# Kernel optimization log

Measured on AMD Instinct MI355X. Metric: run time of the kernel, lower is better.

## Reference

```python
import math
import jax, jax.numpy as jnp
import numpy as np

N = 2048          # batch size
D = 256           # embedding_dim
MEM = 16384       # memory_size
ANOMALY_WEIGHT = 1.0
TEMP = 0.1
MOMENTUM = 0.01
NCLS = 2          # binary phishing labels -> max(labels.max()+1, 2) == 2


def setup_inputs() -> dict:
    key = jax.random.key(0)
    ks = jax.random.split(key, 10)
    s = 1.0 / math.sqrt(D)  # nn.Linear default init range
    return {
        'z': jax.random.normal(ks[0], (N, D), jnp.float32),
        'labels': jax.random.randint(ks[1], (N,), 0, NCLS),
        'memory': jax.random.normal(ks[2], (MEM, D), jnp.float32),
        'memory_weights': jax.random.uniform(ks[3], (MEM,), jnp.float32),
        'running_mean': jnp.zeros((D,), jnp.float32),
        'running_cov': jnp.eye(D, dtype=jnp.float32),
        'Wq': jax.random.uniform(ks[4], (D, D), jnp.float32, -s, s),
        'bq': jax.random.uniform(ks[5], (D,), jnp.float32, -s, s),
        'Wk': jax.random.uniform(ks[6], (D, D), jnp.float32, -s, s),
        'bk': jax.random.uniform(ks[7], (D,), jnp.float32, -s, s),
        'Wv': jax.random.uniform(ks[8], (D, D), jnp.float32, -s, s),
        'bv': jax.random.uniform(ks[9], (D,), jnp.float32, -s, s),
    }


def reference(z, labels, memory, memory_weights, running_mean, running_cov,
              Wq, bq, Wk, bk, Wv, bv):
    # ---- update(z.detach(), labels): entire update path is detached in torch ----
    z_sg = jax.lax.stop_gradient(z)

    # _update_stats: EMA of batch mean / covariance (done before importance)
    mu = z_sg.mean(axis=0)                                  # [D]
    zc = z_sg - mu
    cov = zc.T @ zc / max(N - 1, 1)                         # [D, D]
    rm = (1.0 - MOMENTUM) * running_mean + MOMENTUM * mu
    rc = (1.0 - MOMENTUM) * running_cov + MOMENTUM * cov

    # _mahalanobis with updated running stats
    c = z_sg - rm
    cov_inv = jnp.linalg.inv(rc + 1e-6 * jnp.eye(D, dtype=rc.dtype))
    dist = jnp.sqrt(jnp.clip(jnp.einsum('nd,de,ne->n', c, cov_inv, c), 1e-8))
    a_norm = (dist - dist.min()) / (dist.max() - dist.min() + 1e-8)

    # _mi_proxy: KL(batch label dist || uniform), broadcast to all items
    counts = jnp.zeros((NCLS,), z.dtype).at[labels].add(1.0)
    p = counts / jnp.clip(counts.sum(), 1.0)
    # p / uniform == p * NCLS; clip inside log for safety (both classes present)
    kl = jnp.clip((p * jnp.log(jnp.clip(p * NCLS, 1e-8))).sum(), 0.0)
    importance = (1.0 + ANOMALY_WEIGHT * a_norm) * kl       # [N]

    # serial top-1 priority-queue eviction, in descending-importance order
    order = jnp.argsort(-importance)
    z_ord = z_sg[order]
    imp_ord = importance[order]

    def evict_step(state, inp):
        mem, w = state
        zi, imp = inp
        j = jnp.argmin(w)                   # weakest memory slot
        rep = imp > w[j]
        mem = mem.at[j].set(jnp.where(rep, zi, mem[j]))
        w = w.at[j].set(jnp.where(rep, imp, w[j]))
        return (mem, w), None

    (mem, _), _ = jax.lax.scan(evict_step, (memory, memory_weights), (z_ord, imp_ord))

    # ---- query(z): cross-attention over the (full) updated memory ----
    Q = z @ Wq.T + bq                       # [N, D]
    K = mem @ Wk.T + bk                     # [MEM, D]
    V = mem @ Wv.T + bv                     # [MEM, D]
    sc = (Q @ K.T) / math.sqrt(D)           # [N, MEM]
    attn = jax.nn.softmax(sc / TEMP, axis=-1)
    return z + 0.5 * (attn @ V)
```

## Files before the change

kernel.cpp:

```cpp
#include <hip/hip_runtime.h>
#include <math.h>

#define NB   2048
#define DE   256
#define MEMN 16384
#define CAND_CAP 256
#define FSPL 16
#define FKPS 1024
#define FIT  16

typedef __attribute__((ext_vector_type(8)))  short  short8;
typedef __attribute__((ext_vector_type(16))) float  float16;
typedef __attribute__((ext_vector_type(4)))  unsigned uint4v;
typedef __attribute__((ext_vector_type(2)))  unsigned uint2v;

static const size_t OFF_QB   = 0;
static const size_t OFF_KB   = 262144;
static const size_t OFF_VTB  = 2359296;
static const size_t OFF_LP   = 4456448;
static const size_t OFF_OPB  = 4521984;
static const size_t SO_A    = 0;
static const size_t SO_X    = 65536;
static const size_t SO_MUP  = 131072;
static const size_t SO_DIST = 147456;

__device__ inline unsigned short f2bf(float f) {
  unsigned u = __float_as_uint(f);
  unsigned r = (u + 0x7fffu + ((u >> 16) & 1u)) >> 16;
  return (unsigned short)r;
}
__device__ inline float bf2f(unsigned short s) {
  return __uint_as_float((unsigned)s << 16);
}

__device__ inline unsigned cvtpk_bf16(float lo, float hi) {
  unsigned r;
  asm("v_cvt_pk_bf16_f32 %0, %1, %2" : "=v"(r) : "v"(lo), "v"(hi));
  return r;
}

__device__ inline void halfswap(unsigned& lo, unsigned& hi, int h) {
#if __has_builtin(__builtin_amdgcn_permlane32_swap)
  (void)h;
  uint2v r = __builtin_amdgcn_permlane32_swap(lo, hi, false, false);
  lo = r.x; hi = r.y;
#else
  unsigned a = (unsigned)__shfl_xor((int)lo, 32, 64);
  unsigned b = (unsigned)__shfl_xor((int)hi, 32, 64);
  unsigned nlo = (h == 0) ? lo : b;
  unsigned nhi = (h == 0) ? a  : hi;
  lo = nlo; hi = nhi;
#endif
}

__device__ inline void bitonic_sort_u64(unsigned long long* key, int n, int tid, int nth) {
  for (int k = 2; k <= n; k <<= 1) {
    for (int j = k >> 1; j > 0; j >>= 1) {
      __syncthreads();
      for (int i = tid; i < n; i += nth) {
        int ixj = i ^ j;
        if (ixj > i) {
          unsigned long long a = key[i], b = key[ixj];
          bool up = ((i & k) == 0);
          if ((a > b) == up) { key[i] = b; key[ixj] = a; }
        }
      }
    }
  }
  __syncthreads();
}

__global__ __launch_bounds__(256) void mupart_kernel(const float* __restrict__ z,
                                                     float* __restrict__ mup,
                                                     float* __restrict__ Az) {
  int d = threadIdx.x;
  int r0 = blockIdx.x * 32;
  float4 zero4 = {0.f, 0.f, 0.f, 0.f};
  *(float4*)&Az[(size_t)blockIdx.x * 1024 + threadIdx.x * 4] = zero4;
  float s = 0.f;
  for (int r = 0; r < 32; ++r) s += z[(size_t)(r0 + r) * DE + d];
  mup[blockIdx.x * DE + d] = s;
}

__global__ __launch_bounds__(256) void covpart_kernel(const float* __restrict__ z,
                                                      float* __restrict__ A) {
  __shared__ float As[16][68];
  __shared__ float Bs[16][68];
  int tid = threadIdx.x, tx = tid & 15, ty = tid >> 4;
  int i0 = blockIdx.x * 64, j0 = blockIdx.y * 64;
  int nbase = blockIdx.z * 128;
  float acc[4][4] = {};
  for (int nt = 0; nt < 8; ++nt) {
    int n0 = nbase + nt * 16;
    for (int e = tid; e < 1024; e += 256) {
      int c = e & 63, nn = e >> 6;
      As[nn][c] = z[(size_t)(n0 + nn) * DE + i0 + c];
      Bs[nn][c] = z[(size_t)(n0 + nn) * DE + j0 + c];
    }
    __syncthreads();
#pragma unroll
    for (int nn = 0; nn < 16; ++nn) {
      float4 a4 = *(const float4*)&As[nn][ty * 4];
      float4 b4 = *(const float4*)&Bs[nn][tx * 4];
      acc[0][0] += a4.x*b4.x; acc[0][1] += a4.x*b4.y; acc[0][2] += a4.x*b4.z; acc[0][3] += a4.x*b4.w;
      acc[1][0] += a4.y*b4.x; acc[1][1] += a4.y*b4.y; acc[1][2] += a4.y*b4.z; acc[1][3] += a4.y*b4.w;
      acc[2][0] += a4.z*b4.x; acc[2][1] += a4.z*b4.y; acc[2][2] += a4.z*b4.z; acc[2][3] += a4.z*b4.w;
      acc[3][0] += a4.w*b4.x; acc[3][1] += a4.w*b4.y; acc[3][2] += a4.w*b4.z; acc[3][3] += a4.w*b4.w;
    }
    __syncthreads();
  }
  for (int r = 0; r < 4; ++r) {
    int i = i0 + ty * 4 + r;
    for (int c = 0; c < 4; ++c) {
      int j = j0 + tx * 4 + c;
      atomicAdd(&A[(size_t)i * DE + j], acc[r][c]);
    }
  }
}

__global__ __launch_bounds__(256) void gemmx_kernel(const float* __restrict__ ZtZ,
                                                    const float* __restrict__ rcov,
                                                    const float* __restrict__ mup,
                                                    float* __restrict__ X) {
  __shared__ float Ea[16][17];
  __shared__ float Eb[16][17];
  __shared__ float mus[256];
  int t = threadIdx.x, tx = t & 15, ty = t >> 4;
  int i0 = blockIdx.x * 16, j0 = blockIdx.y * 16;
  {
    float s = 0.f;
    for (int b = 0; b < 64; ++b) s += mup[b * DE + t];
    mus[t] = s;
  }
  __syncthreads();
  const float c1 = 0.01f / (float)(NB - 1);
  const float invN = 1.0f / (float)NB;
  float acc = 0.f;
  for (int k0 = 0; k0 < 256; k0 += 16) {
    int c = k0 + tx;
    {
      int r = i0 + ty;
      float base = 0.99f * rcov[(size_t)r * DE + c] +
                   c1 * (ZtZ[(size_t)r * DE + c] - mus[r] * mus[c] * invN);
      float e = -base;
      if (r == c) e += 1.0f - 1e-6f;
      Ea[ty][tx] = e;
    }
    {
      int r = j0 + ty;
      float base = 0.99f * rcov[(size_t)r * DE + c] +
                   c1 * (ZtZ[(size_t)r * DE + c] - mus[r] * mus[c] * invN);
      float e = -base;
      if (r == c) e += 1.0f - 1e-6f;
      Eb[ty][tx] = e;
    }
    __syncthreads();
#pragma unroll
    for (int k = 0; k < 16; ++k) acc += Ea[ty][k] * Eb[tx][k];
    __syncthreads();
  }
  int r = i0 + ty, c = j0 + tx;
  float base = 0.99f * rcov[(size_t)r * DE + c] +
               c1 * (ZtZ[(size_t)r * DE + c] - mus[r] * mus[c] * invN);
  float e = -base;
  if (r == c) e += 1.0f - 1e-6f;
  X[(size_t)r * DE + c] = acc + e + ((r == c) ? 1.0f : 0.0f);
}

__global__ __launch_bounds__(256) void dist_kernel(const float* __restrict__ z,
                                                   const float* __restrict__ rmean,
                                                   const float* __restrict__ mup,
                                                   const float* __restrict__ X,
                                                   float* __restrict__ dist) {
  __shared__ float cc[4][256];
  __shared__ float4 red[256];
  int n0 = blockIdx.x * 4, i = threadIdx.x;
  float s = 0.f;
  for (int b = 0; b < 64; ++b) s += mup[b * DE + i];
  float rmi = 0.99f * rmean[i] + 0.01f * s * (1.0f / (float)NB);
#pragma unroll
  for (int r = 0; r < 4; ++r) cc[r][i] = z[(size_t)(n0 + r) * DE + i] - rmi;
  __syncthreads();
  float y0 = 0.f, y1 = 0.f, y2 = 0.f, y3 = 0.f;
#pragma unroll 8
  for (int j = 0; j < DE; ++j) {
    float x = X[(size_t)j * DE + i];
    y0 += x * cc[0][j]; y1 += x * cc[1][j]; y2 += x * cc[2][j]; y3 += x * cc[3][j];
  }
  float4 v;
  v.x = y0 * cc[0][i]; v.y = y1 * cc[1][i]; v.z = y2 * cc[2][i]; v.w = y3 * cc[3][i];
  red[i] = v;
  __syncthreads();
  for (int sH = 128; sH > 0; sH >>= 1) {
    if (i < sH) {
      float4 a = red[i], b = red[i + sH];
      a.x += b.x; a.y += b.y; a.z += b.z; a.w += b.w;
      red[i] = a;
    }
    __syncthreads();
  }
  if (i < 4) {
    float4 tt = red[0];
    float d = (i == 0) ? tt.x : (i == 1) ? tt.y : (i == 2) ? tt.z : tt.w;
    dist[n0 + i] = sqrtf(fmaxf(d, 1e-8f));
  }
}

__global__ __launch_bounds__(1024) void update_kernel(const float* __restrict__ dist,
                                                      const int* __restrict__ labels,
                                                      const float* __restrict__ weights,
                                                      const float* __restrict__ z,
                                                      float* __restrict__ memory) {
  __shared__ unsigned long long ikeys[NB];
  __shared__ unsigned long long ck[CAND_CAP];
  __shared__ unsigned long long gmin[16];
  __shared__ int slots[CAND_CAP], srcs[CAND_CAP];
  __shared__ float smin[16], smax[16];
  __shared__ int scnt[16];
  __shared__ float s_kl, s_dmin, s_inv;
  __shared__ int s_ccnt, s_m, s_stop, s_bg;
  int t = threadIdx.x;
  int wid = t >> 6, lane = t & 63;

  float mn = 1e30f, mx = -1e30f; int c1 = 0;
  for (int n = t; n < NB; n += 1024) {
    float d = dist[n];
    mn = fminf(mn, d); mx = fmaxf(mx, d);
    c1 += labels[n];
  }
#pragma unroll
  for (int o = 32; o > 0; o >>= 1) {
    mn = fminf(mn, __shfl_xor(mn, o, 64));
    mx = fmaxf(mx, __shfl_xor(mx, o, 64));
    c1 += __shfl_xor(c1, o, 64);
  }
  if (lane == 0) { smin[wid] = mn; smax[wid] = mx; scnt[wid] = c1; }
  if (t == 0) { s_ccnt = 0; s_m = 0; s_stop = 0; }
  __syncthreads();
  if (t == 0) {
    float a = 1e30f, b = -1e30f; int cc = 0;
    for (int i = 0; i < 16; ++i) { a = fminf(a, smin[i]); b = fmaxf(b, smax[i]); cc += scnt[i]; }
    float p1 = (float)cc / (float)NB;
    float p0 = (float)(NB - cc) / (float)NB;
    float kl = p0 * logf(fmaxf(2.f * p0, 1e-8f)) + p1 * logf(fmaxf(2.f * p1, 1e-8f));
    s_kl = fmaxf(kl, 0.f);
    s_dmin = a;
    s_inv = 1.0f / (b - a + 1e-8f);
  }
  __syncthreads();
  float kl = s_kl;

  for (int n = t; n < NB; n += 1024) {
    float imp = (1.0f + (dist[n] - s_dmin) * s_inv) * kl;
    ikeys[n] = ((unsigned long long)(unsigned)(~__float_as_uint(imp)) << 32) | (unsigned)n;
  }
  float thresh = 2.f * kl;
  for (int j = t; j < MEMN; j += 1024) {
    float wv = weights[j];
    if (wv < thresh) {
      int p = atomicAdd(&s_ccnt, 1);
      if (p < CAND_CAP) ck[p] = ((unsigned long long)__float_as_uint(wv) << 32) | (unsigned)j;
    }
  }
  __syncthreads();
  int C = s_ccnt; if (C > CAND_CAP) C = CAND_CAP;
  for (int i = t; i < CAND_CAP; i += 1024)
    if (i >= C) ck[i] = 0xFFFFFFFFFFFFFFFFULL;
  bitonic_sort_u64(ck, CAND_CAP, t, 1024);

  {
    unsigned long long a = ikeys[wid * 128 + lane];
    unsigned long long b = ikeys[wid * 128 + 64 + lane];
    unsigned long long mm = a < b ? a : b;
#pragma unroll
    for (int o = 32; o > 0; o >>= 1) {
      unsigned long long ot = (unsigned long long)__shfl_xor((long long)mm, o, 64);
      if (ot < mm) mm = ot;
    }
    if (lane == 0) gmin[wid] = mm;
  }
  __syncthreads();

  float prevv = 0.f;
  for (int i = 0; i < C; ++i) {
    if (t == 0) {
      unsigned long long best = 0xFFFFFFFFFFFFFFFFULL;
      for (int g = 0; g < 16; ++g) if (gmin[g] < best) best = gmin[g];
      float im = __uint_as_float(~(unsigned)(best >> 32));
      float wv = __uint_as_float((unsigned)(ck[i] >> 32));
      bool ok = (im > wv) && (i == 0 || prevv >= wv);
      if (ok) {
        int idx = (int)(best & 0xffffffffULL);
        slots[s_m] = (int)(ck[i] & 0xffffffffULL);
        srcs[s_m]  = idx;
        s_m++;
        prevv = im;
        ikeys[idx] = 0xFFFFFFFFFFFFFFFFULL;
        s_bg = idx >> 7;
      } else {
        s_stop = 1; s_bg = -1;
      }
    }
    __syncthreads();
    if (s_stop) break;
    if (wid == s_bg) {
      unsigned long long a = ikeys[wid * 128 + lane];
      unsigned long long b = ikeys[wid * 128 + 64 + lane];
      unsigned long long mm = a < b ? a : b;
#pragma unroll
      for (int o = 32; o > 0; o >>= 1) {
        unsigned long long ot = (unsigned long long)__shfl_xor((long long)mm, o, 64);
        if (ot < mm) mm = ot;
      }
      if (lane == 0) gmin[wid] = mm;
    }
    __syncthreads();
  }
  int m = s_m;
  for (int e = t; e < m * DE; e += 1024) {
    int i = e >> 8, d = e & 255;
    memory[(size_t)slots[i] * DE + d] = z[(size_t)srcs[i] * DE + d];
  }
}

__global__ __launch_bounds__(256, 1) void qkv_kernel(
    const float* __restrict__ z, const float* __restrict__ memory,
    const float* __restrict__ Wq, const float* __restrict__ bq,
    const float* __restrict__ Wk, const float* __restrict__ bk,
    const float* __restrict__ Wv, const float* __restrict__ bv,
    unsigned short* __restrict__ Qbf, unsigned short* __restrict__ Kbf,
    unsigned short* __restrict__ Vtb) {
  __shared__ unsigned short Bsh[64 * 264];
  int flat = blockIdx.x;
  const float *Af, *Bf, *bias;
  unsigned short* C;
  int bias_row, vtile, gx, gy, ldC;
  if (flat < 64) {
    gx = flat & 15; gy = flat >> 4;
    Af = z; Bf = Wq; bias = bq; bias_row = 0; vtile = 0; C = Qbf; ldC = DE;
  } else if (flat < 576) {
    int f = flat - 64; gx = f & 127; gy = f >> 7;
    Af = memory; Bf = Wk; bias = bk; bias_row = 0; vtile = 0; C = Kbf; ldC = DE;
  } else {
    int f = flat - 576; gx = f & 1; gy = f >> 1;
    Af = Wv; Bf = memory; bias = bv; bias_row = 1; vtile = 1; C = Vtb; ldC = 0;
  }

  int tid = threadIdx.x;
  int w = tid >> 6, lane = tid & 63;
  int m = lane & 31, h = lane >> 5;
  int arow = gx * 128 + w * 32 + m;
  int n0 = gy * 64;

  short8 af[16];
#pragma unroll
  for (int kc = 0; kc < 16; ++kc) {
    const float* src = &Af[(size_t)arow * DE + kc * 16 + h * 8];
    float4 f0 = *(const float4*)&src[0];
    float4 f1 = *(const float4*)&src[4];
    short8 v;
    v[0] = (short)f2bf(f0.x); v[1] = (short)f2bf(f0.y);
    v[2] = (short)f2bf(f0.z); v[3] = (short)f2bf(f0.w);
    v[4] = (short)f2bf(f1.x); v[5] = (short)f2bf(f1.y);
    v[6] = (short)f2bf(f1.z); v[7] = (short)f2bf(f1.w);
    af[kc] = v;
  }
  {
    int r = tid >> 2, q = tid & 3;
    const float* src = &Bf[(size_t)(n0 + r) * DE + q * 64];
    unsigned short* dst = &Bsh[r * 264 + q * 64];
#pragma unroll
    for (int j = 0; j < 8; ++j) {
      float4 f0 = *(const float4*)&src[j * 8];
      float4 f1 = *(const float4*)&src[j * 8 + 4];
      short8 v;
      v[0] = (short)f2bf(f0.x); v[1] = (short)f2bf(f0.y);
      v[2] = (short)f2bf(f0.z); v[3] = (short)f2bf(f0.w);
      v[4] = (short)f2bf(f1.x); v[5] = (short)f2bf(f1.y);
      v[6] = (short)f2bf(f1.z); v[7] = (short)f2bf(f1.w);
      *(short8*)&dst[j * 8] = v;
    }
  }
  __syncthreads();

  float16 a0 = {}, a1 = {};
#pragma unroll
  for (int kc = 0; kc < 16; ++kc) {
    short8 b0 = *(const short8*)&Bsh[(0 * 32 + m) * 264 + kc * 16 + h * 8];
    short8 b1 = *(const short8*)&Bsh[(1 * 32 + m) * 264 + kc * 16 + h * 8];
    a0 = __builtin_amdgcn_mfma_f32_32x32x16_bf16(af[kc], b0, a0, 0, 0, 0);
    a1 = __builtin_amdgcn_mfma_f32_32x32x16_bf16(af[kc], b1, a1, 0, 0, 0);
  }
#pragma unroll
  for (int r = 0; r < 16; ++r) {
    int rr = (r & 3) + 8 * (r >> 2) + 4 * h;
    int orow = gx * 128 + w * 32 + rr;
    int oc0 = n0 + m, oc1 = n0 + 32 + m;
    float bb0 = bias_row ? bias[orow] : bias[oc0];
    float bb1 = bias_row ? bias[orow] : bias[oc1];
    if (!vtile) {
      C[(size_t)orow * ldC + oc0] = f2bf(a0[r] + bb0);
      C[(size_t)orow * ldC + oc1] = f2bf(a1[r] + bb1);
    } else {
      C[(size_t)(oc0 >> 5) * 8192 + (size_t)orow * 32 + (oc0 & 31)] = f2bf(a0[r] + bb0);
      C[(size_t)(oc1 >> 5) * 8192 + (size_t)orow * 32 + (oc1 & 31)] = f2bf(a1[r] + bb1);
    }
  }
}

__global__ __launch_bounds__(512, 2) void flash_kernel(
    const unsigned short* __restrict__ Qb, const unsigned short* __restrict__ Kb,
    const unsigned short* __restrict__ Vtb, unsigned short* __restrict__ Opb,
    float* __restrict__ Lp) {
  __shared__ unsigned short Ks[64 * 264];
  __shared__ unsigned short Vs[256 * 40];

  int tid = threadIdx.x;
  int w = tid >> 6, lane = tid & 63;
  int m = lane & 31, h = lane >> 5;
  int sp = blockIdx.x, qg = blockIdx.y, dh = blockIdx.z;
  int myrow = qg * 256 + w * 32 + m;

  short8 qf[16];
#pragma unroll
  for (int kc = 0; kc < 16; ++kc)
    qf[kc] = *(const short8*)&Qb[(size_t)myrow * DE + kc * 16 + h * 8];

  float16 O[4] = {};
  float lacc = 0.f;

  short8 kreg[4], vreg[2];
#define LOAD_TILES(kb_)                                                              \
  {                                                                                  \
    int kb = (kb_);                                                                  \
    _Pragma("unroll")                                                                \
    for (int i = 0; i < 4; ++i) {                                                    \
      int c = i * 512 + tid, kr = c >> 5, kcol = c & 31;                             \
      kreg[i] = *(const short8*)&Kb[(size_t)(kb + kr) * DE + kcol * 8];              \
    }                                                                                \
    const unsigned short* vg = &Vtb[(size_t)((kb) >> 5) * 8192 + (size_t)dh * 4096]; \
    _Pragma("unroll")                                                                \
    for (int i = 0; i < 2; ++i) {                                                    \
      int c = i * 512 + tid;                                                         \
      int sub = c >> 9, cc = c & 511;                                                \
      vreg[i] = *(const short8*)&vg[(size_t)sub * 8192 + cc * 8];                    \
    }                                                                                \
  }
#define STORE_TILES()                                                                \
  {                                                                                  \
    _Pragma("unroll")                                                                \
    for (int i = 0; i < 4; ++i) {                                                    \
      int c = i * 512 + tid, kr = c >> 5, kcol = c & 31;                             \
      *(short8*)&Ks[kr * 264 + kcol * 8] = kreg[i];                                  \
    }                                                                                \
    _Pragma("unroll")                                                                \
    for (int i = 0; i < 2; ++i) {                                                    \
      int c = i * 512 + tid, dr = c >> 2, dc = c & 3;                                \
      *(short8*)&Vs[dr * 40 + dc * 8] = vreg[i];                                     \
    }                                                                                \
  }

  LOAD_TILES(sp * FKPS);

  for (int it = 0; it < FIT; ++it) {
    __syncthreads();
    STORE_TILES();
    if (it + 1 < FIT) LOAD_TILES(sp * FKPS + (it + 1) * 64);
    __syncthreads();

#pragma unroll
    for (int sub = 0; sub < 2; ++sub) {
      float16 s0 = {}, s1 = {};
      __builtin_amdgcn_s_setprio(1);
#pragma unroll
      for (int kc = 0; kc < 16; kc += 2) {
        short8 b0 = *(const short8*)&Ks[(sub * 32 + m) * 264 + kc * 16 + h * 8];
        short8 b1 = *(const short8*)&Ks[(sub * 32 + m) * 264 + (kc + 1) * 16 + h * 8];
        s0 = __builtin_amdgcn_mfma_f32_32x32x16_bf16(b0, qf[kc], s0, 0, 0, 0);
        s1 = __builtin_amdgcn_mfma_f32_32x32x16_bf16(b1, qf[kc + 1], s1, 0, 0, 0);
      }
      __builtin_amdgcn_s_setprio(0);

      float p[16];
#pragma unroll
      for (int r = 0; r < 16; ++r)
        p[r] = exp2f(fmaf(s0[r] + s1[r], 0.90168440f, -16.0f));

      lacc += ((p[0] + p[1]) + (p[2] + p[3])) + ((p[4] + p[5]) + (p[6] + p[7])) +
              ((p[8] + p[9]) + (p[10] + p[11])) + ((p[12] + p[13]) + (p[14] + p[15]));

      unsigned c0 = cvtpk_bf16(p[0],  p[1]);
      unsigned c1 = cvtpk_bf16(p[2],  p[3]);
      unsigned c2 = cvtpk_bf16(p[4],  p[5]);
      unsigned c3 = cvtpk_bf16(p[6],  p[7]);
      unsigned c4 = cvtpk_bf16(p[8],  p[9]);
      unsigned c5 = cvtpk_bf16(p[10], p[11]);
      unsigned c6 = cvtpk_bf16(p[12], p[13]);
      unsigned c7 = cvtpk_bf16(p[14], p[15]);
      halfswap(c0, c2, h);
      halfswap(c1, c3, h);
      halfswap(c4, c6, h);
      halfswap(c5, c7, h);
      uint4v w0v = {c0, c1, c2, c3};
      uint4v w1v = {c4, c5, c6, c7};
      short8 pa0 = __builtin_bit_cast(short8, w0v);
      short8 pa1 = __builtin_bit_cast(short8, w1v);

      __builtin_amdgcn_s_setprio(1);
#pragma unroll
      for (int ct = 0; ct < 4; ++ct) {
        short8 vb0 = *(const short8*)&Vs[(sub * 128 + ct * 32 + m) * 40 + h * 8];
        short8 vb1 = *(const short8*)&Vs[(sub * 128 + ct * 32 + m) * 40 + 16 + h * 8];
        O[ct] = __builtin_amdgcn_mfma_f32_32x32x16_bf16(pa0, vb0, O[ct], 0, 0, 0);
        O[ct] = __builtin_amdgcn_mfma_f32_32x32x16_bf16(pa1, vb1, O[ct], 0, 0, 0);
      }
      __builtin_amdgcn_s_setprio(0);
    }
  }
#undef LOAD_TILES
#undef STORE_TILES

  size_t ob = ((size_t)sp * NB + qg * 256 + w * 32) * DE + dh * 128;
#pragma unroll
  for (int ct = 0; ct < 4; ++ct)
#pragma unroll
    for (int r = 0; r < 16; ++r) {
      int rr = (r & 3) + 8 * (r >> 2) + 4 * h;
      Opb[ob + (size_t)rr * DE + ct * 32 + m] = f2bf(O[ct][r]);
    }
  float ltot = lacc + __shfl_xor(lacc, 32, 64);
  if (dh == 0 && h == 0)
    Lp[sp * NB + qg * 256 + w * 32 + m] = ltot;
}

__global__ __launch_bounds__(256) void combine_kernel(const float* __restrict__ z,
                                                      const unsigned short* __restrict__ Opb,
                                                      const float* __restrict__ Lp,
                                                      float* __restrict__ out) {
  int n = blockIdx.x, c = threadIdx.x;
  float num = 0.f, den = 0.f;
#pragma unroll
  for (int s = 0; s < FSPL; ++s) {
    den += Lp[s * NB + n];
    num += bf2f(Opb[((size_t)s * NB + n) * DE + c]);
  }
  size_t base = (size_t)n * DE + c;
  out[base] = z[base] + 0.5f * num / den;
}

extern "C" void kernel_launch(void* const* d_in, const int* in_sizes, int n_in,
                              void* d_out, int out_size, void* d_ws, size_t ws_size,
                              hipStream_t stream) {
  (void)in_sizes; (void)n_in; (void)out_size; (void)ws_size;
  const float* z       = (const float*)d_in[0];
  const int*   labels  = (const int*)d_in[1];
  float*       memory  = (float*)d_in[2];
  const float* weights = (const float*)d_in[3];
  const float* rmean   = (const float*)d_in[4];
  const float* rcov    = (const float*)d_in[5];
  const float* Wq      = (const float*)d_in[6];
  const float* bq      = (const float*)d_in[7];
  const float* Wk      = (const float*)d_in[8];
  const float* bk      = (const float*)d_in[9];
  const float* Wv      = (const float*)d_in[10];
  const float* bv      = (const float*)d_in[11];
  float* out = (float*)d_out;
  float* ws  = (float*)d_ws;

  unsigned short* Qbf = (unsigned short*)(ws + OFF_QB);
  unsigned short* Kbf = (unsigned short*)(ws + OFF_KB);
  unsigned short* Vtb = (unsigned short*)(ws + OFF_VTB);
  float* Lp           = ws + OFF_LP;
  unsigned short* Opb = (unsigned short*)(ws + OFF_OPB);
  float* SB    = ws + OFF_OPB;
  float* A     = SB + SO_A;
  float* X     = SB + SO_X;
  float* mup   = SB + SO_MUP;
  float* dist  = SB + SO_DIST;

  mupart_kernel<<<64, 256, 0, stream>>>(z, mup, A);
  covpart_kernel<<<dim3(4, 4, 16), 256, 0, stream>>>(z, A);
  gemmx_kernel<<<dim3(16, 16), 256, 0, stream>>>(A, rcov, mup, X);
  dist_kernel<<<NB / 4, 256, 0, stream>>>(z, rmean, mup, X, dist);
  update_kernel<<<1, 1024, 0, stream>>>(dist, labels, weights, z, memory);
  qkv_kernel<<<1088, 256, 0, stream>>>(z, memory, Wq, bq, Wk, bk, Wv, bv, Qbf, Kbf, Vtb);
  flash_kernel<<<dim3(FSPL, NB / 256, 2), 512, 0, stream>>>(Qbf, Kbf, Vtb, Opb, Lp);
  combine_kernel<<<NB, 256, 0, stream>>>(z, Opb, Lp, out);
}
```

Measured before the change: 255.7 us.

## Drop head-dim split in flash kernel to avoid recomputing QK scores

The flash attention kernel no longer splits the V/output head dimension across two blocks. Before, both blocks recomputed the same QK^T scores and exponentials. Each block now handles all 256 output columns over 32-key tiles, and the key range is split into 32 parts instead of 16, so the block count stays the same. The cost is more accumulator registers per thread, which risks spills or lower occupancy, and twice as many partial outputs for the combine kernel to read.

```diff
diff --git a/kernel.cpp b/kernel.cpp
--- a/kernel.cpp
+++ b/kernel.cpp
@@ -5,8 +5,8 @@
 #define DE   256
 #define MEMN 16384
 #define CAND_CAP 256
-#define FSPL 16
-#define FKPS 1024
+#define FSPL 32
+#define FKPS 512
 #define FIT  16
 
 typedef __attribute__((ext_vector_type(8)))  short  short8;
@@ -412,13 +412,13 @@
     const unsigned short* __restrict__ Qb, const unsigned short* __restrict__ Kb,
     const unsigned short* __restrict__ Vtb, unsigned short* __restrict__ Opb,
     float* __restrict__ Lp) {
-  __shared__ unsigned short Ks[64 * 264];
+  __shared__ unsigned short Ks[32 * 264];
   __shared__ unsigned short Vs[256 * 40];
 
   int tid = threadIdx.x;
   int w = tid >> 6, lane = tid & 63;
   int m = lane & 31, h = lane >> 5;
-  int sp = blockIdx.x, qg = blockIdx.y, dh = blockIdx.z;
+  int sp = blockIdx.x, qg = blockIdx.y;
   int myrow = qg * 256 + w * 32 + m;
 
   short8 qf[16];
@@ -426,30 +426,29 @@
   for (int kc = 0; kc < 16; ++kc)
     qf[kc] = *(const short8*)&Qb[(size_t)myrow * DE + kc * 16 + h * 8];
 
-  float16 O[4] = {};
+  float16 O[8] = {};
   float lacc = 0.f;
 
-  short8 kreg[4], vreg[2];
+  short8 kreg[2], vreg[2];
 #define LOAD_TILES(kb_)                                                              \
   {                                                                                  \
     int kb = (kb_);                                                                  \
     _Pragma("unroll")                                                                \
-    for (int i = 0; i < 4; ++i) {                                                    \
+    for (int i = 0; i < 2; ++i) {                                                    \
       int c = i * 512 + tid, kr = c >> 5, kcol = c & 31;                             \
       kreg[i] = *(const short8*)&Kb[(size_t)(kb + kr) * DE + kcol * 8];              \
     }                                                                                \
-    const unsigned short* vg = &Vtb[(size_t)((kb) >> 5) * 8192 + (size_t)dh * 4096]; \
+    const unsigned short* vg = &Vtb[(size_t)((kb) >> 5) * 8192];                     \
     _Pragma("unroll")                                                                \
     for (int i = 0; i < 2; ++i) {                                                    \
       int c = i * 512 + tid;                                                         \
-      int sub = c >> 9, cc = c & 511;                                                \
-      vreg[i] = *(const short8*)&vg[(size_t)sub * 8192 + cc * 8];                    \
+      vreg[i] = *(const short8*)&vg[c * 8];                                          \
     }                                                                                \
   }
 #define STORE_TILES()                                                                \
   {                                                                                  \
     _Pragma("unroll")                                                                \
-    for (int i = 0; i < 4; ++i) {                                                    \
+    for (int i = 0; i < 2; ++i) {                                                    \
       int c = i * 512 + tid, kr = c >> 5, kcol = c & 31;                             \
       *(short8*)&Ks[kr * 264 + kcol * 8] = kreg[i];                                  \
     }                                                                                \
@@ -465,71 +464,66 @@
   for (int it = 0; it < FIT; ++it) {
     __syncthreads();
     STORE_TILES();
-    if (it + 1 < FIT) LOAD_TILES(sp * FKPS + (it + 1) * 64);
-    __syncthreads();
-
-#pragma unroll
-    for (int sub = 0; sub < 2; ++sub) {
-      float16 s0 = {}, s1 = {};
-      __builtin_amdgcn_s_setprio(1);
-#pragma unroll
-      for (int kc = 0; kc < 16; kc += 2) {
-        short8 b0 = *(const short8*)&Ks[(sub * 32 + m) * 264 + kc * 16 + h * 8];
-        short8 b1 = *(const short8*)&Ks[(sub * 32 + m) * 264 + (kc + 1) * 16 + h * 8];
-        s0 = __builtin_amdgcn_mfma_f32_32x32x16_bf16(b0, qf[kc], s0, 0, 0, 0);
-        s1 = __builtin_amdgcn_mfma_f32_32x32x16_bf16(b1, qf[kc + 1], s1, 0, 0, 0);
-      }
-      __builtin_amdgcn_s_setprio(0);
-
-      float p[16];
-#pragma unroll
-      for (int r = 0; r < 16; ++r)
-        p[r] = exp2f(fmaf(s0[r] + s1[r], 0.90168440f, -16.0f));
-
-      lacc += ((p[0] + p[1]) + (p[2] + p[3])) + ((p[4] + p[5]) + (p[6] + p[7])) +
-              ((p[8] + p[9]) + (p[10] + p[11])) + ((p[12] + p[13]) + (p[14] + p[15]));
-
-      unsigned c0 = cvtpk_bf16(p[0],  p[1]);
-      unsigned c1 = cvtpk_bf16(p[2],  p[3]);
-      unsigned c2 = cvtpk_bf16(p[4],  p[5]);
-      unsigned c3 = cvtpk_bf16(p[6],  p[7]);
-      unsigned c4 = cvtpk_bf16(p[8],  p[9]);
-      unsigned c5 = cvtpk_bf16(p[10], p[11]);
-      unsigned c6 = cvtpk_bf16(p[12], p[13]);
-      unsigned c7 = cvtpk_bf16(p[14], p[15]);
-      halfswap(c0, c2, h);
-      halfswap(c1, c3, h);
-      halfswap(c4, c6, h);
-      halfswap(c5, c7, h);
-      uint4v w0v = {c0, c1, c2, c3};
-      uint4v w1v = {c4, c5, c6, c7};
-      short8 pa0 = __builtin_bit_cast(short8, w0v);
-      short8 pa1 = __builtin_bit_cast(short8, w1v);
-
-      __builtin_amdgcn_s_setprio(1);
-#pragma unroll
-      for (int ct = 0; ct < 4; ++ct) {
-        short8 vb0 = *(const short8*)&Vs[(sub * 128 + ct * 32 + m) * 40 + h * 8];
-        short8 vb1 = *(const short8*)&Vs[(sub * 128 + ct * 32 + m) * 40 + 16 + h * 8];
-        O[ct] = __builtin_amdgcn_mfma_f32_32x32x16_bf16(pa0, vb0, O[ct], 0, 0, 0);
-        O[ct] = __builtin_amdgcn_mfma_f32_32x32x16_bf16(pa1, vb1, O[ct], 0, 0, 0);
-      }
-      __builtin_amdgcn_s_setprio(0);
-    }
+    if (it + 1 < FIT) LOAD_TILES(sp * FKPS + (it + 1) * 32);
+    __syncthreads();
+
+    float16 s = {};
+    __builtin_amdgcn_s_setprio(1);
+#pragma unroll
+    for (int kc = 0; kc < 16; ++kc) {
+      short8 b0 = *(const short8*)&Ks[m * 264 + kc * 16 + h * 8];
+      s = __builtin_amdgcn_mfma_f32_32x32x16_bf16(b0, qf[kc], s, 0, 0, 0);
+    }
+    __builtin_amdgcn_s_setprio(0);
+
+    float p[16];
+#pragma unroll
+    for (int r = 0; r < 16; ++r)
+      p[r] = exp2f(fmaf(s[r], 0.90168440f, -16.0f));
+
+    lacc += ((p[0] + p[1]) + (p[2] + p[3])) + ((p[4] + p[5]) + (p[6] + p[7])) +
+            ((p[8] + p[9]) + (p[10] + p[11])) + ((p[12] + p[13]) + (p[14] + p[15]));
+
+    unsigned c0 = cvtpk_bf16(p[0],  p[1]);
+    unsigned c1 = cvtpk_bf16(p[2],  p[3]);
+    unsigned c2 = cvtpk_bf16(p[4],  p[5]);
+    unsigned c3 = cvtpk_bf16(p[6],  p[7]);
+    unsigned c4 = cvtpk_bf16(p[8],  p[9]);
+    unsigned c5 = cvtpk_bf16(p[10], p[11]);
+    unsigned c6 = cvtpk_bf16(p[12], p[13]);
+    unsigned c7 = cvtpk_bf16(p[14], p[15]);
+    halfswap(c0, c2, h);
+    halfswap(c1, c3, h);
+    halfswap(c4, c6, h);
+    halfswap(c5, c7, h);
+    uint4v w0v = {c0, c1, c2, c3};
+    uint4v w1v = {c4, c5, c6, c7};
+    short8 pa0 = __builtin_bit_cast(short8, w0v);
+    short8 pa1 = __builtin_bit_cast(short8, w1v);
+
+    __builtin_amdgcn_s_setprio(1);
+#pragma unroll
+    for (int ct = 0; ct < 8; ++ct) {
+      short8 vb0 = *(const short8*)&Vs[(ct * 32 + m) * 40 + h * 8];
+      short8 vb1 = *(const short8*)&Vs[(ct * 32 + m) * 40 + 16 + h * 8];
+      O[ct] = __builtin_amdgcn_mfma_f32_32x32x16_bf16(pa0, vb0, O[ct], 0, 0, 0);
+      O[ct] = __builtin_amdgcn_mfma_f32_32x32x16_bf16(pa1, vb1, O[ct], 0, 0, 0);
+    }
+    __builtin_amdgcn_s_setprio(0);
   }
 #undef LOAD_TILES
 #undef STORE_TILES
 
-  size_t ob = ((size_t)sp * NB + qg * 256 + w * 32) * DE + dh * 128;
-#pragma unroll
-  for (int ct = 0; ct < 4; ++ct)
+  size_t ob = ((size_t)sp * NB + qg * 256 + w * 32) * DE;
+#pragma unroll
+  for (int ct = 0; ct < 8; ++ct)
 #pragma unroll
     for (int r = 0; r < 16; ++r) {
       int rr = (r & 3) + 8 * (r >> 2) + 4 * h;
       Opb[ob + (size_t)rr * DE + ct * 32 + m] = f2bf(O[ct][r]);
     }
   float ltot = lacc + __shfl_xor(lacc, 32, 64);
-  if (dh == 0 && h == 0)
+  if (h == 0)
     Lp[sp * NB + qg * 256 + w * 32 + m] = ltot;
 }
 
@@ -584,6 +578,6 @@
   dist_kernel<<<NB / 4, 256, 0, stream>>>(z, rmean, mup, X, dist);
   update_kernel<<<1, 1024, 0, stream>>>(dist, labels, weights, z, memory);
   qkv_kernel<<<1088, 256, 0, stream>>>(z, memory, Wq, bq, Wk, bk, Wv, bv, Qbf, Kbf, Vtb);
-  flash_kernel<<<dim3(FSPL, NB / 256, 2), 512, 0, stream>>>(Qbf, Kbf, Vtb, Opb, Lp);
+  flash_kernel<<<dim3(FSPL, NB / 256), 512, 0, stream>>>(Qbf, Kbf, Vtb, Opb, Lp);
   combine_kernel<<<NB, 256, 0, stream>>>(z, Opb, Lp, out);
 }
```

Result: faster. 241.4 us (-5.6%).
